# Performance work log

Hardware: AMD Instinct MI355X
Metric: run time of the kernel (lower is better)

Reference implementation:

```python
import jax, jax.numpy as jnp
import numpy as np

N = 8192
C = 256


def setup_inputs() -> dict:
    key = jax.random.key(0)
    k_x, k_wr, k_br, k_wc, k_bc = jax.random.split(key, 5)
    scale = 1.0 / np.sqrt(C)
    return {
        "x": jax.random.normal(k_x, (N, C), dtype=jnp.float32),
        "w_reduce": jax.random.uniform(k_wr, (C, C), dtype=jnp.float32, minval=-scale, maxval=scale),
        "b_reduce": jax.random.uniform(k_br, (C,), dtype=jnp.float32, minval=-scale, maxval=scale),
        "w_contr": jax.random.uniform(k_wc, (1, C), dtype=jnp.float32, minval=-scale, maxval=scale),
        "b_contr": jax.random.uniform(k_bc, (1,), dtype=jnp.float32, minval=-scale, maxval=scale),
    }


def reference(x, w_reduce, b_reduce, w_contr, b_contr):
    # Original math: y_ij = reduce(x_i + x_j); z_ij = sigmoid(contr(y_ij));
    # out_i = mean_j y_ij * z_ij.
    # Since reduce/contr are affine, decompose without the [N,N,C] tensor:
    #   y_ij = r_i + r_j + b_reduce,        r = x @ Wr^T
    #   contr(y_ij) = s_i + s_j + c0,       s = r . wc, c0 = b_reduce . wc + bc
    n = x.shape[0]
    r = x @ w_reduce.T                                   # [N, C]
    wc = w_contr[0]                                      # [C]
    s = r @ wc                                           # [N]
    c0 = b_reduce @ wc + b_contr[0]                      # scalar
    Z = jax.nn.sigmoid(s[:, None] + s[None, :] + c0)     # [N, N] pairwise gate
    m = jnp.mean(Z, axis=1, keepdims=True)               # [N, 1]
    # mean_j (r_i + r_j + b) * z_ij = (r_i + b) * m_i + (Z @ r)_i / N
    out = (r + b_reduce) * m + (Z @ r) / n               # [N, C]
    return out
```

## Files before the change

kernel.cpp:

```cpp
#include <hip/hip_runtime.h>
#include <hip/hip_bf16.h>
#include <stdint.h>

#define NN 8192
#define CC 256
#define NSPLIT 8
#define JR (NN / NSPLIT)
#define NITER (JR / 32)

typedef float f32x4 __attribute__((ext_vector_type(4)));
typedef float f32x2 __attribute__((ext_vector_type(2)));
typedef short s16x8 __attribute__((ext_vector_type(8)));

#define LOG2E 1.4426950408889634f

#define OFF_WT  0
#define OFF_R   (OFF_WT + CC*CC)
#define OFF_S2  (OFF_R + NN*CC)
#define OFF_C0  (OFF_S2 + NN)
#define OFF_SS  (OFF_C0 + 16)
#define OFF_V   (OFF_SS + NSPLIT*NN)
#define OFF_RB  (OFF_V + (NSPLIT*NN*CC)/2)

__global__ __launch_bounds__(256) void k_prep(const float* __restrict__ w,
                                              const float* __restrict__ br,
                                              const float* __restrict__ wcv,
                                              const float* __restrict__ bc,
                                              float* __restrict__ ws) {
  int k = blockIdx.x, c = threadIdx.x;
  ws[OFF_WT + k * CC + c] = w[c * CC + k];
  if (blockIdx.x == 0 && threadIdx.x < 64) {
    int lane = threadIdx.x;
    f32x4 b4 = *(const f32x4*)&br[lane * 4];
    f32x4 w4 = *(const f32x4*)&wcv[lane * 4];
    float d = b4[0]*w4[0] + b4[1]*w4[1] + b4[2]*w4[2] + b4[3]*w4[3];
    #pragma unroll
    for (int m = 32; m >= 1; m >>= 1) d += __shfl_xor(d, m, 64);
    if (lane == 0) { ws[OFF_C0] = d + bc[0]; ws[OFF_C0 + 1] = (d + bc[0]) * LOG2E; }
  }
}

__global__ __launch_bounds__(256) void k_r(const float* __restrict__ x,
                                           float* __restrict__ ws) {
  __shared__ float xs[64][260];
  int bi = blockIdx.x;
  int rowblk = bi >> 2, colblk = bi & 3;
  int tid = threadIdx.x;
  int i0 = rowblk * 64;
  for (int t = tid; t < 64 * 64; t += 256) {
    int rr = t >> 6, c4 = t & 63;
    *(f32x4*)&xs[rr][c4 * 4] = *(const f32x4*)&x[(i0 + rr) * CC + c4 * 4];
  }
  __syncthreads();
  int tx = tid & 15, ty = tid >> 4;
  int cbase = colblk * 64 + tx * 4;
  int r0 = ty * 4;
  float acc[4][4] = {};
  const float* wt = ws + OFF_WT;
  for (int k = 0; k < CC; k += 2) {
    f32x4 wv0 = *(const f32x4*)&wt[k * CC + cbase];
    f32x4 wv1 = *(const f32x4*)&wt[(k + 1) * CC + cbase];
    f32x2 xv[4];
    #pragma unroll
    for (int rr = 0; rr < 4; rr++) xv[rr] = *(const f32x2*)&xs[r0 + rr][k];
    #pragma unroll
    for (int rr = 0; rr < 4; rr++)
      #pragma unroll
      for (int cc = 0; cc < 4; cc++)
        acc[rr][cc] = fmaf(xv[rr][1], wv1[cc], fmaf(xv[rr][0], wv0[cc], acc[rr][cc]));
  }
  #pragma unroll
  for (int rr = 0; rr < 4; rr++) {
    f32x4 o = {acc[rr][0], acc[rr][1], acc[rr][2], acc[rr][3]};
    *(f32x4*)&ws[OFF_R + (size_t)(i0 + r0 + rr) * CC + cbase] = o;
  }
  unsigned long long* rb64 = (unsigned long long*)(ws + OFF_RB);
  int j0r = i0 + r0;
  #pragma unroll
  for (int cc = 0; cc < 4; cc++) {
    int c = cbase + cc;
    unsigned long long v = 0;
    #pragma unroll
    for (int rr = 0; rr < 4; rr++) {
      unsigned u = __float_as_uint(acc[rr][cc]);
      u = (u + 0x7fffu + ((u >> 16) & 1u)) >> 16;
      v |= (unsigned long long)u << (16 * rr);
    }
    int us = (((j0r >> 5) * 16 + (c >> 4)) * 64 + (((j0r >> 3) & 3) * 16 + (c & 15))) * 8 + (j0r & 7);
    rb64[us >> 2] = v;
  }
}

__global__ __launch_bounds__(256) void k_s(const float* __restrict__ wcv,
                                           float* __restrict__ ws) {
  int tid = threadIdx.x;
  int lane = tid & 63;
  int row = blockIdx.x * 4 + (tid >> 6);
  f32x4 rv = *(const f32x4*)&ws[OFF_R + (size_t)row * CC + lane * 4];
  f32x4 wv = *(const f32x4*)&wcv[lane * 4];
  float d = rv[0]*wv[0] + rv[1]*wv[1] + rv[2]*wv[2] + rv[3]*wv[3];
  #pragma unroll
  for (int m = 32; m >= 1; m >>= 1) d += __shfl_xor(d, m, 64);
  if (lane == 0) ws[OFF_S2 + row] = d * LOG2E;
}


#define STAGE(BUF, IT) { \
  const char* gb_ = rbase + (size_t)(IT) * 16384 + w * 1024 + l * 16; \
  _Pragma("unroll") \
  for (int q_ = 0; q_ < 4; q_++) \
    __builtin_amdgcn_global_load_lds( \
      (const __attribute__((address_space(1))) void*)(gb_ + q_ * 4096), \
      (__attribute__((address_space(3))) void*)&ldsb[(BUF) * 16384 + w * 1024 + q_ * 4096], \
      16, 0, 0); }

#define WAITBAR4 { asm volatile("s_waitcnt vmcnt(4)" ::: "memory"); \
  __builtin_amdgcn_s_barrier(); \
  __builtin_amdgcn_sched_barrier(0); }

#define WAITBAR0 { asm volatile("s_waitcnt vmcnt(0)" ::: "memory"); \
  __builtin_amdgcn_s_barrier(); \
  __builtin_amdgcn_sched_barrier(0); }

#define SB0 __builtin_amdgcn_sched_barrier(0);

#define SIGMOID(IT, AFA, AFB) { \
  f32x4 sj0_ = *(const f32x4*)&s2l[(IT) * 32 + g * 8]; \
  f32x4 sj1_ = *(const f32x4*)&s2l[(IT) * 32 + g * 8 + 4]; \
  _Pragma("unroll") \
  for (int t_ = 0; t_ < 8; t_++) { \
    float sj_ = (t_ < 4) ? sj0_[t_] : sj1_[t_ - 4]; \
    float eA_, eB_; \
    asm("v_exp_f32 %0, %1" : "=v"(eA_) : "v"(negaA - sj_)); \
    asm("v_exp_f32 %0, %1" : "=v"(eB_) : "v"(negaB - sj_)); \
    float zA_ = __builtin_amdgcn_rcpf(1.0f + eA_); \
    float zB_ = __builtin_amdgcn_rcpf(1.0f + eB_); \
    unsigned uA_ = __float_as_uint(zA_); \
    uA_ = (uA_ + 0x7fffu + ((uA_ >> 16) & 1u)) >> 16; \
    (AFA)[t_] = (short)uA_; \
    unsigned uB_ = __float_as_uint(zB_); \
    uB_ = (uB_ + 0x7fffu + ((uB_ >> 16) & 1u)) >> 16; \
    (AFB)[t_] = (short)uB_; } }

#define MFMA_PHASE(AFA, AFB, LP) { \
  __builtin_amdgcn_s_setprio(1); \
  _Pragma("unroll") \
  for (int ct_ = 0; ct_ < 16; ct_++) { \
    s16x8 bf_ = *(const s16x8*)((LP) + ct_ * 1024 + l * 16); \
    accA[ct_] = __builtin_amdgcn_mfma_f32_16x16x32_bf16(AFA, bf_, accA[ct_], 0, 0, 0); \
    accB[ct_] = __builtin_amdgcn_mfma_f32_16x16x32_bf16(AFB, bf_, accB[ct_], 0, 0, 0); } \
  acc1A = __builtin_amdgcn_mfma_f32_16x16x32_bf16(AFA, ones, acc1A, 0, 0, 0); \
  acc1B = __builtin_amdgcn_mfma_f32_16x16x32_bf16(AFB, ones, acc1B, 0, 0, 0); \
  __builtin_amdgcn_s_setprio(0); }

__global__ __launch_bounds__(256, 2) void k_main(float* __restrict__ ws) {
  __shared__ char ldsb[3 * 16384];
  __shared__ float s2l[1024];
  int blk = blockIdx.x;
  int rt = blk >> 3, h = blk & 7;
  int tid = threadIdx.x;
  int w = tid >> 6, l = tid & 63;
  int lr = l & 15, g = l >> 4;
  int iw = rt * 128 + w * 32;
  float c02 = ws[OFF_C0 + 1];
  float negaA = -(ws[OFF_S2 + iw + lr] + c02);
  float negaB = -(ws[OFF_S2 + iw + 16 + lr] + c02);

  const float* s2p = ws + OFF_S2 + h * JR;
  *(f32x4*)&s2l[tid * 4] = *(const f32x4*)(s2p + tid * 4);
  __syncthreads();

  f32x4 accA[16], accB[16], acc1A, acc1B;
  #pragma unroll
  for (int i = 0; i < 16; i++) { accA[i] = (f32x4)(0.f); accB[i] = (f32x4)(0.f); }
  acc1A = (f32x4)(0.f); acc1B = (f32x4)(0.f);
  s16x8 ones;
  #pragma unroll
  for (int t = 0; t < 8; t++) ones[t] = (short)0x3F80;

  const char* rbase = (const char*)(ws + OFF_RB) + (size_t)h * (JR * CC * 2);

  STAGE(0, 0);
  STAGE(1, 1);
  s16x8 afA0, afB0, afA1, afB1;
  SIGMOID(0, afA0, afB0);

  int sA = 0;
  #pragma unroll 1
  for (int J = 0; J < NITER - 2; J += 2) {
    int sB = sA + 1; if (sB == 3) sB = 0;
    int sC = sB + 1; if (sC == 3) sC = 0;

    WAITBAR4;
    STAGE(sC, J + 2);
    SB0;
    SIGMOID(J + 1, afA1, afB1);
    MFMA_PHASE(afA0, afB0, ldsb + sA * 16384);

    WAITBAR4;
    STAGE(sA, J + 3);
    SB0;
    SIGMOID(J + 2, afA0, afB0);
    MFMA_PHASE(afA1, afB1, ldsb + sB * 16384);

    sA = sC;
  }
  {
    int sB = sA + 1; if (sB == 3) sB = 0;
    WAITBAR4;
    SIGMOID(NITER - 1, afA1, afB1);
    MFMA_PHASE(afA0, afB0, ldsb + sA * 16384);
    WAITBAR0;
    MFMA_PHASE(afA1, afB1, ldsb + sB * 16384);
  }

  if (lr == 0) {
    #pragma unroll
    for (int q = 0; q < 4; q++) {
      ws[OFF_SS + h * NN + iw + g * 4 + q] = acc1A[q];
      ws[OFF_SS + h * NN + iw + 16 + g * 4 + q] = acc1B[q];
    }
  }
  unsigned short* Vb = (unsigned short*)(ws + OFF_V);
  size_t vbase = (size_t)h * (NN * CC);
  #pragma unroll
  for (int ct = 0; ct < 16; ct++) {
    #pragma unroll
    for (int q = 0; q < 4; q++) {
      unsigned uA = __float_as_uint(accA[ct][q]);
      uA = (uA + 0x7fffu + ((uA >> 16) & 1u)) >> 16;
      Vb[vbase + (size_t)(iw + g * 4 + q) * CC + ct * 16 + lr] = (unsigned short)uA;
      unsigned uB = __float_as_uint(accB[ct][q]);
      uB = (uB + 0x7fffu + ((uB >> 16) & 1u)) >> 16;
      Vb[vbase + (size_t)(iw + 16 + g * 4 + q) * CC + ct * 16 + lr] = (unsigned short)uB;
    }
  }
}

__global__ __launch_bounds__(256) void k_epi(const float* __restrict__ br,
                                             const float* __restrict__ ws,
                                             float* __restrict__ out) {
  int idx = blockIdx.x * 256 + threadIdx.x;
  int i = idx >> 5, c8 = (idx & 31) * 8;
  float S = 0.f;
  #pragma unroll
  for (int p = 0; p < NSPLIT; p++) S += ws[OFF_SS + p * NN + i];
  float m = S * (1.0f / NN);
  float v[8] = {};
  const unsigned short* Vb = (const unsigned short*)(ws + OFF_V);
  #pragma unroll
  for (int p = 0; p < NSPLIT; p++) {
    s16x8 pv = *(const s16x8*)&Vb[(size_t)p * (NN * CC) + (size_t)i * CC + c8];
    #pragma unroll
    for (int t = 0; t < 8; t++)
      v[t] += __uint_as_float(((unsigned)(unsigned short)pv[t]) << 16);
  }
  f32x4 r0 = *(const f32x4*)&ws[OFF_R + (size_t)i * CC + c8];
  f32x4 r1 = *(const f32x4*)&ws[OFF_R + (size_t)i * CC + c8 + 4];
  f32x4 b0 = *(const f32x4*)&br[c8];
  f32x4 b1 = *(const f32x4*)&br[c8 + 4];
  f32x4 o0, o1;
  #pragma unroll
  for (int t = 0; t < 4; t++) {
    o0[t] = (r0[t] + b0[t]) * m + v[t] * (1.0f / NN);
    o1[t] = (r1[t] + b1[t]) * m + v[t + 4] * (1.0f / NN);
  }
  *(f32x4*)&out[(size_t)i * CC + c8] = o0;
  *(f32x4*)&out[(size_t)i * CC + c8 + 4] = o1;
}

extern "C" void kernel_launch(void* const* d_in, const int* in_sizes, int n_in,
                              void* d_out, int out_size, void* d_ws, size_t ws_size,
                              hipStream_t stream) {
  const float* x  = (const float*)d_in[0];
  const float* w  = (const float*)d_in[1];
  const float* br = (const float*)d_in[2];
  const float* wc = (const float*)d_in[3];
  const float* bc = (const float*)d_in[4];
  float* ws = (float*)d_ws;
  float* out = (float*)d_out;
  (void)in_sizes; (void)n_in; (void)out_size; (void)ws_size;

  k_prep<<<256, 256, 0, stream>>>(w, br, wc, bc, ws);
  k_r<<<512, 256, 0, stream>>>(x, ws);
  k_s<<<2048, 256, 0, stream>>>(wc, ws);
  k_main<<<512, 256, 0, stream>>>(ws);
  k_epi<<<1024, 256, 0, stream>>>(br, ws, out);
}
```

Before: 84.08 us.

## Fuse s computation into r GEMM, truncate sigmoid bf16, move sigmoid before barrier

The separate k_s kernel, which re-read r from global memory, is replaced by partial dot products with wc computed in the k_r epilogue. These partials are written per column block and summed by a tiny k_s2 kernel. The sigmoid-to-bf16 conversion now truncates instead of rounding to nearest-even, which trims ALU work in the hot loop but adds a small bias. The sigmoid computation is moved before the wait/barrier so it can overlap with outstanding loads.

New measurement: 87.85 us. +4.5%, slower.

```diff
diff --git a/kernel.cpp b/kernel.cpp
--- a/kernel.cpp
+++ b/kernel.cpp
@@ -19,7 +19,8 @@
 #define OFF_S2  (OFF_R + NN*CC)
 #define OFF_C0  (OFF_S2 + NN)
 #define OFF_SS  (OFF_C0 + 16)
-#define OFF_V   (OFF_SS + NSPLIT*NN)
+#define OFF_SP  (OFF_SS + NSPLIT*NN)
+#define OFF_V   (OFF_SP + 4*NN)
 #define OFF_RB  (OFF_V + (NSPLIT*NN*CC)/2)
 
 __global__ __launch_bounds__(256) void k_prep(const float* __restrict__ w,
@@ -41,6 +42,7 @@
 }
 
 __global__ __launch_bounds__(256) void k_r(const float* __restrict__ x,
+                                           const float* __restrict__ wcv,
                                            float* __restrict__ ws) {
   __shared__ float xs[64][260];
   int bi = blockIdx.x;
@@ -89,19 +91,26 @@
     int us = (((j0r >> 5) * 16 + (c >> 4)) * 64 + (((j0r >> 3) & 3) * 16 + (c & 15))) * 8 + (j0r & 7);
     rb64[us >> 2] = v;
   }
-}
-
-__global__ __launch_bounds__(256) void k_s(const float* __restrict__ wcv,
-                                           float* __restrict__ ws) {
-  int tid = threadIdx.x;
-  int lane = tid & 63;
-  int row = blockIdx.x * 4 + (tid >> 6);
-  f32x4 rv = *(const f32x4*)&ws[OFF_R + (size_t)row * CC + lane * 4];
-  f32x4 wv = *(const f32x4*)&wcv[lane * 4];
-  float d = rv[0]*wv[0] + rv[1]*wv[1] + rv[2]*wv[2] + rv[3]*wv[3];
-  #pragma unroll
-  for (int m = 32; m >= 1; m >>= 1) d += __shfl_xor(d, m, 64);
-  if (lane == 0) ws[OFF_S2 + row] = d * LOG2E;
+  f32x4 wc4 = *(const f32x4*)&wcv[cbase];
+  float sd[4];
+  #pragma unroll
+  for (int rr = 0; rr < 4; rr++) {
+    sd[rr] = acc[rr][0]*wc4[0] + acc[rr][1]*wc4[1] + acc[rr][2]*wc4[2] + acc[rr][3]*wc4[3];
+    #pragma unroll
+    for (int m = 1; m < 16; m <<= 1) sd[rr] += __shfl_xor(sd[rr], m, 64);
+  }
+  if (tx == 0) {
+    #pragma unroll
+    for (int rr = 0; rr < 4; rr++)
+      ws[OFF_SP + colblk * NN + j0r + rr] = sd[rr];
+  }
+}
+
+__global__ __launch_bounds__(256) void k_s2(float* __restrict__ ws) {
+  int row = blockIdx.x * 256 + threadIdx.x;
+  float s = ws[OFF_SP + row] + ws[OFF_SP + NN + row]
+          + ws[OFF_SP + 2 * NN + row] + ws[OFF_SP + 3 * NN + row];
+  ws[OFF_S2 + row] = s * LOG2E;
 }
 
 
@@ -135,12 +144,8 @@
     asm("v_exp_f32 %0, %1" : "=v"(eB_) : "v"(negaB - sj_)); \
     float zA_ = __builtin_amdgcn_rcpf(1.0f + eA_); \
     float zB_ = __builtin_amdgcn_rcpf(1.0f + eB_); \
-    unsigned uA_ = __float_as_uint(zA_); \
-    uA_ = (uA_ + 0x7fffu + ((uA_ >> 16) & 1u)) >> 16; \
-    (AFA)[t_] = (short)uA_; \
-    unsigned uB_ = __float_as_uint(zB_); \
-    uB_ = (uB_ + 0x7fffu + ((uB_ >> 16) & 1u)) >> 16; \
-    (AFB)[t_] = (short)uB_; } }
+    (AFA)[t_] = (short)(__float_as_uint(zA_) >> 16); \
+    (AFB)[t_] = (short)(__float_as_uint(zB_) >> 16); } }
 
 #define MFMA_PHASE(AFA, AFB, LP) { \
   __builtin_amdgcn_s_setprio(1); \
@@ -191,26 +196,28 @@
     int sB = sA + 1; if (sB == 3) sB = 0;
     int sC = sB + 1; if (sC == 3) sC = 0;
 
+    SIGMOID(J + 1, afA1, afB1);
     WAITBAR4;
     STAGE(sC, J + 2);
     SB0;
-    SIGMOID(J + 1, afA1, afB1);
     MFMA_PHASE(afA0, afB0, ldsb + sA * 16384);
 
+    SIGMOID(J + 2, afA0, afB0);
     WAITBAR4;
     STAGE(sA, J + 3);
     SB0;
-    SIGMOID(J + 2, afA0, afB0);
     MFMA_PHASE(afA1, afB1, ldsb + sB * 16384);
 
     sA = sC;
   }
   {
     int sB = sA + 1; if (sB == 3) sB = 0;
+    SIGMOID(NITER - 1, afA1, afB1);
     WAITBAR4;
-    SIGMOID(NITER - 1, afA1, afB1);
+    SB0;
     MFMA_PHASE(afA0, afB0, ldsb + sA * 16384);
     WAITBAR0;
+    SB0;
     MFMA_PHASE(afA1, afB1, ldsb + sB * 16384);
   }
 
@@ -282,8 +289,8 @@
   (void)in_sizes; (void)n_in; (void)out_size; (void)ws_size;
 
   k_prep<<<256, 256, 0, stream>>>(w, br, wc, bc, ws);
-  k_r<<<512, 256, 0, stream>>>(x, ws);
-  k_s<<<2048, 256, 0, stream>>>(wc, ws);
+  k_r<<<512, 256, 0, stream>>>(x, wc, ws);
+  k_s2<<<32, 256, 0, stream>>>(ws);
   k_main<<<512, 256, 0, stream>>>(ws);
   k_epi<<<1024, 256, 0, stream>>>(br, ws, out);
 }
```
